# Optimization experiments

Hardware: AMD Instinct MI355X
Metric: run time of the kernel (lower is better)

Reference implementation:

```python
import jax, jax.numpy as jnp
import numpy as np

BEV_H, BEV_W = 50, 50
D_PILLAR = 4
PC = (-51.2, -51.2, -5.0, 51.2, 51.2, 3.0)
S_IMG = 518.0   # input_size; also img H and W used for uv normalization
LN_EPS = 1e-5
FUSE_EPS = 1e-6
C_CTX = 256


def _layernorm(x):
    mu = jnp.mean(x, axis=-1, keepdims=True)
    var = jnp.mean((x - mu) ** 2, axis=-1, keepdims=True)
    return (x - mu) * jax.lax.rsqrt(var + LN_EPS)


def _make_lidar2img(V):
    # realistic surround-view cameras: yaw-rotated extrinsics + pinhole intrinsics
    fx = fy = 400.0
    cx = cy = S_IMG / 2.0
    K = np.array([[fx, 0, cx, 0], [0, fy, cy, 0], [0, 0, 1, 0], [0, 0, 0, 1]], dtype=np.float64)
    mats = []
    for v in range(V):
        th = 2.0 * np.pi * v / V
        f = np.array([np.cos(th), np.sin(th), 0.0])      # camera forward (z)
        l = np.array([-np.sin(th), np.cos(th), 0.0])     # camera x (lateral)
        d = np.array([0.0, 0.0, -1.0])                   # camera y (down)
        R = np.stack([l, d, f], axis=0)
        t = np.array([0.0, 0.0, 1.5])                    # camera position in lidar frame
        E = np.eye(4); E[:3, :3] = R; E[:3, 3] = -R @ t
        mats.append(K @ E)
    return np.stack(mats, axis=0).astype(np.float32)     # (V,4,4)


def setup_inputs() -> dict:
    key = jax.random.key(0)
    k1, = jax.random.split(key, 1)
    B, V, N, C = 1, 6, 37 * 37, 768
    last_tokens = jax.random.normal(k1, (B, V, N, C), dtype=jnp.float32)
    lidar2img = jnp.asarray(_make_lidar2img(V))[None]    # (B,V,4,4)
    return {
        "last_tokens": last_tokens,
        "lidar2img": lidar2img,
        "w_view": jnp.zeros((1, V, 1), dtype=jnp.float32),
        "post_gamma": jnp.ones((C,), dtype=jnp.float32),
        "post_beta": jnp.zeros((C,), dtype=jnp.float32),
        "logits": jnp.zeros((C_CTX, C // C_CTX), dtype=jnp.float32),
        "patch_h": 37,
        "patch_w": 37,
    }


def _projection(lidar2img, dtype):
    # BEVFormer-style 3d reference points -> per-camera uv + visibility mask
    Z = int(round(PC[5] - PC[2]))  # 8
    zs = (jnp.linspace(0.5, Z - 0.5, D_PILLAR, dtype=dtype) / Z)[:, None, None]
    xs = (jnp.linspace(0.5, BEV_W - 0.5, BEV_W, dtype=dtype) / BEV_W)[None, None, :]
    ys = (jnp.linspace(0.5, BEV_H - 0.5, BEV_H, dtype=dtype) / BEV_H)[None, :, None]
    x, y, z = jnp.broadcast_arrays(xs, ys, zs)           # (D,H,W) each
    ref = jnp.stack([x, y, z], axis=-1).reshape(D_PILLAR, BEV_H * BEV_W, 3)
    ref = ref * jnp.array([PC[3] - PC[0], PC[4] - PC[1], PC[5] - PC[2]], dtype) \
        + jnp.array([PC[0], PC[1], PC[2]], dtype)
    ref4 = jnp.concatenate([ref, jnp.ones_like(ref[..., :1])], axis=-1)  # (D,Q,4)
    pts = jnp.einsum('bvij,dqj->bdvqi', lidar2img, ref4)  # (B,D,V,Q,4)
    zc = pts[..., 2]
    valid = zc > 1e-5
    uv = pts[..., :2] / jnp.maximum(zc, 1e-5)[..., None] / S_IMG
    u, v = uv[..., 0], uv[..., 1]
    valid = valid & (u > 0.0) & (u < 1.0) & (v > 0.0) & (v < 1.0)
    # -> (B,V,Q,D)
    tr = lambda a: jnp.transpose(a, (0, 2, 3, 1))
    return tr(u), tr(v), tr(valid)


def reference(last_tokens, lidar2img, w_view, post_gamma, post_beta, logits, patch_h, patch_w):
    B, V, N, C = last_tokens.shape
    Hp, Wp = int(patch_h), int(patch_w)
    Q = BEV_H * BEV_W
    dt = last_tokens.dtype

    # pre-LN over channels (no affine)
    tok = _layernorm(last_tokens)                         # (B,V,N,C)

    u, v, valid = _projection(lidar2img, dt)              # (B,V,Q,D)
    u, v = jax.lax.stop_gradient(u), jax.lax.stop_gradient(v)  # torch: @no_grad

    # pixel coords on the patch grid (align_corners=True grid_sample equivalent)
    x_p = (u * S_IMG + 0.5) / S_IMG * Wp - 0.5
    y_p = (v * S_IMG + 0.5) / S_IMG * Hp - 0.5

    x0 = jnp.floor(x_p); fx = x_p - x0; x0 = x0.astype(jnp.int32)
    y0 = jnp.floor(y_p); fy = y_p - y0; y0 = y0.astype(jnp.int32)

    QD = Q * D_PILLAR
    acc = jnp.zeros((B, V, QD, C), dtype=dt)
    for dx in (0, 1):
        for dy in (0, 1):
            xi, yi = x0 + dx, y0 + dy
            inb = (xi >= 0) & (xi < Wp) & (yi >= 0) & (yi < Hp)  # zeros padding
            w = jnp.where(dx, fx, 1.0 - fx) * jnp.where(dy, fy, 1.0 - fy) * inb.astype(dt)
            idx = jnp.clip(yi, 0, Hp - 1) * Wp + jnp.clip(xi, 0, Wp - 1)
            g = jnp.take_along_axis(tok, idx.reshape(B, V, QD, 1), axis=2)  # (B,V,QD,C)
            acc = acc + w.reshape(B, V, QD, 1) * g
    sampled = acc.reshape(B, V, Q, D_PILLAR, C)

    m = valid.astype(dt)                                  # (B,V,Q,D)
    feat = jnp.einsum('bvqdc,bvqd->bvqc', sampled, m)     # mask-weighted sum over pillar pts
    cnt = jnp.sum(m, axis=-1)                             # (B,V,Q)

    wv = jax.nn.softplus(w_view)                          # (1,V,1) positive per-view weights
    num = jnp.sum(feat * wv[..., None], axis=1)           # (B,Q,C)
    den = jnp.sum(cnt * wv, axis=1)                       # (B,Q)
    fused = num / (den[..., None] + FUSE_EPS)

    h = _layernorm(fused) * post_gamma + post_beta        # post-LN with affine

    g = C // C_CTX
    wg = jax.nn.softmax(logits, axis=-1)                  # (C_CTX, g)
    y = jnp.sum(h.reshape(B, Q, C_CTX, g) * wg[None, None], axis=-1)  # (B,Q,C_CTX)

    return jnp.transpose(y.reshape(B, BEV_H, BEV_W, C_CTX), (0, 3, 1, 2))
```

## Files before the change

### kernel.cpp

```cpp
#include <hip/hip_runtime.h>
#include <math.h>

#define NV      6
#define ND      4
#define NQ      2500
#define NPATCH  1369
#define NROWS   (NV * NPATCH)
#define CTOK    768
#define HP      37
#define WP      37
#define CCTX    256
#define QT      4
#define MAXM    96

__device__ __forceinline__ float softplus_f(float x) {
    return (x > 20.0f) ? x : log1pf(expf(x));
}

__global__ __launch_bounds__(256) void ln_stats_kernel(
    const float* __restrict__ tok, float* __restrict__ stats )
{
    const int wave = threadIdx.x >> 6, lane = threadIdx.x & 63;
    const int row = blockIdx.x * 4 + wave;
    if (row >= NROWS) return;
    const float4* x = (const float4*)(tok + (size_t)row * CTOK);
    float s = 0.f, ss = 0.f;
    #pragma unroll
    for (int i = 0; i < 3; ++i) {
        float4 v = x[lane + 64 * i];
        s  += (v.x + v.y) + (v.z + v.w);
        ss += v.x * v.x + v.y * v.y + v.z * v.z + v.w * v.w;
    }
    #pragma unroll
    for (int off = 32; off; off >>= 1) {
        s  += __shfl_down(s,  off, 64);
        ss += __shfl_down(ss, off, 64);
    }
    if (lane == 0) {
        float mu  = s * (1.0f / (float)CTOK);
        float var = ss * (1.0f / (float)CTOK) - mu * mu;
        float rs  = rsqrtf(fmaxf(var, 0.0f) + 1e-5f);
        stats[row * 2 + 0] = mu;
        stats[row * 2 + 1] = rs;
    }
}

__global__ __launch_bounds__(256) void bev_fuse_kernel(
    const float* __restrict__ tok,
    const float* __restrict__ stats,
    const float* __restrict__ lidar2img,
    const float* __restrict__ w_view,
    const float* __restrict__ gamma,
    const float* __restrict__ beta,
    const float* __restrict__ logits,
    float* __restrict__ out)
{
    __shared__ float s_b[QT][MAXM];
    __shared__ float s_bmu[QT][MAXM];
    __shared__ int   s_idx[QT][MAXM];
    __shared__ float s_den[QT][NV * ND];
    __shared__ int   s_cnt[QT];
    __shared__ float s_y[QT][CCTX];

    const int t = threadIdx.x;
    const int q0 = blockIdx.x * QT;

    if (t < QT) s_cnt[t] = 0;
    __syncthreads();

    if (t < QT * NV * ND) {
        const int qi = t / 24;
        const int p  = t - qi * 24;
        const int v = p >> 2, d = p & 3;
        const int q = q0 + qi;
        const int qy = q / 50, qx = q - qy * 50;
        float xf = ((float)qx + 0.5f) * (1.0f / 50.0f);
        float yf = ((float)qy + 0.5f) * (1.0f / 50.0f);
        float zf = (0.5f + (float)d * (7.0f / 3.0f)) * (1.0f / 8.0f);
        float X = xf * 102.4f - 51.2f;
        float Y = yf * 102.4f - 51.2f;
        float Z = zf * 8.0f - 5.0f;
        const float* M = lidar2img + v * 16;
        float px = M[0] * X + M[1] * Y + M[2]  * Z + M[3];
        float py = M[4] * X + M[5] * Y + M[6]  * Z + M[7];
        float pz = M[8] * X + M[9] * Y + M[10] * Z + M[11];
        bool valid = pz > 1e-5f;
        float zc = fmaxf(pz, 1e-5f);
        float uu = px / zc * (1.0f / 518.0f);
        float vv = py / zc * (1.0f / 518.0f);
        valid = valid && (uu > 0.0f) && (uu < 1.0f) && (vv > 0.0f) && (vv < 1.0f);

        float wv = softplus_f(w_view[v]);
        s_den[qi][p] = valid ? wv : 0.0f;

        if (valid) {
            float x_p = (uu * 518.0f + 0.5f) * (37.0f / 518.0f) - 0.5f;
            float y_p = (vv * 518.0f + 0.5f) * (37.0f / 518.0f) - 0.5f;
            float x0f = floorf(x_p), y0f = floorf(y_p);
            float fx = x_p - x0f, fy = y_p - y0f;
            int x0 = (int)x0f, y0 = (int)y0f;
            #pragma unroll
            for (int corner = 0; corner < 4; ++corner) {
                int dx = corner & 1, dy = corner >> 1;
                int xi = x0 + dx, yi = y0 + dy;
                bool inb = (xi >= 0) && (xi < WP) && (yi >= 0) && (yi < HP);
                float w = (dx ? fx : (1.0f - fx)) * (dy ? fy : (1.0f - fy));
                if (inb && w != 0.0f) {
                    int idx = v * NPATCH + yi * WP + xi;
                    float b = w * wv * stats[idx * 2 + 1];
                    int slot = atomicAdd(&s_cnt[qi], 1);
                    s_b[qi][slot]   = b;
                    s_bmu[qi][slot] = b * stats[idx * 2 + 0];
                    s_idx[qi][slot] = idx;
                }
            }
        }
    }
    __syncthreads();

    const int w = t >> 6, lane = t & 63;
    const int m = s_cnt[w];

    float den = 0.0f;
    #pragma unroll
    for (int p = 0; p < NV * ND; ++p) den += s_den[w][p];
    float c0 = 0.0f;
    for (int j = 0; j < m; ++j) c0 += s_bmu[w][j];

    const float4* base = (const float4*)tok;
    const int fp = 3 * lane;
    float4 a0 = {0,0,0,0}, a1 = {0,0,0,0}, a2 = {0,0,0,0};
    int j = 0;
    for (; j + 2 <= m; j += 2) {
        float b0 = s_b[w][j], b1 = s_b[w][j + 1];
        const float4* p0 = base + (size_t)s_idx[w][j]     * (CTOK / 4) + fp;
        const float4* p1 = base + (size_t)s_idx[w][j + 1] * (CTOK / 4) + fp;
        float4 x0 = p0[0], x1 = p0[1], x2 = p0[2];
        float4 y0 = p1[0], y1 = p1[1], y2 = p1[2];
        a0.x = fmaf(b0, x0.x, a0.x); a0.y = fmaf(b0, x0.y, a0.y);
        a0.z = fmaf(b0, x0.z, a0.z); a0.w = fmaf(b0, x0.w, a0.w);
        a1.x = fmaf(b0, x1.x, a1.x); a1.y = fmaf(b0, x1.y, a1.y);
        a1.z = fmaf(b0, x1.z, a1.z); a1.w = fmaf(b0, x1.w, a1.w);
        a2.x = fmaf(b0, x2.x, a2.x); a2.y = fmaf(b0, x2.y, a2.y);
        a2.z = fmaf(b0, x2.z, a2.z); a2.w = fmaf(b0, x2.w, a2.w);
        a0.x = fmaf(b1, y0.x, a0.x); a0.y = fmaf(b1, y0.y, a0.y);
        a0.z = fmaf(b1, y0.z, a0.z); a0.w = fmaf(b1, y0.w, a0.w);
        a1.x = fmaf(b1, y1.x, a1.x); a1.y = fmaf(b1, y1.y, a1.y);
        a1.z = fmaf(b1, y1.z, a1.z); a1.w = fmaf(b1, y1.w, a1.w);
        a2.x = fmaf(b1, y2.x, a2.x); a2.y = fmaf(b1, y2.y, a2.y);
        a2.z = fmaf(b1, y2.z, a2.z); a2.w = fmaf(b1, y2.w, a2.w);
    }
    if (j < m) {
        float b0 = s_b[w][j];
        const float4* p0 = base + (size_t)s_idx[w][j] * (CTOK / 4) + fp;
        float4 x0 = p0[0], x1 = p0[1], x2 = p0[2];
        a0.x = fmaf(b0, x0.x, a0.x); a0.y = fmaf(b0, x0.y, a0.y);
        a0.z = fmaf(b0, x0.z, a0.z); a0.w = fmaf(b0, x0.w, a0.w);
        a1.x = fmaf(b0, x1.x, a1.x); a1.y = fmaf(b0, x1.y, a1.y);
        a1.z = fmaf(b0, x1.z, a1.z); a1.w = fmaf(b0, x1.w, a1.w);
        a2.x = fmaf(b0, x2.x, a2.x); a2.y = fmaf(b0, x2.y, a2.y);
        a2.z = fmaf(b0, x2.z, a2.z); a2.w = fmaf(b0, x2.w, a2.w);
    }

    float f[12];
    {
        float inv = 1.0f / (den + 1e-6f);
        f[0]  = (a0.x - c0) * inv; f[1]  = (a0.y - c0) * inv;
        f[2]  = (a0.z - c0) * inv; f[3]  = (a0.w - c0) * inv;
        f[4]  = (a1.x - c0) * inv; f[5]  = (a1.y - c0) * inv;
        f[6]  = (a1.z - c0) * inv; f[7]  = (a1.w - c0) * inv;
        f[8]  = (a2.x - c0) * inv; f[9]  = (a2.y - c0) * inv;
        f[10] = (a2.z - c0) * inv; f[11] = (a2.w - c0) * inv;
    }

    float s = 0.f, ss = 0.f;
    #pragma unroll
    for (int i = 0; i < 12; ++i) { s += f[i]; ss += f[i] * f[i]; }
    #pragma unroll
    for (int off = 32; off; off >>= 1) {
        s  += __shfl_down(s,  off, 64);
        ss += __shfl_down(ss, off, 64);
    }
    s  = __shfl(s,  0, 64);
    ss = __shfl(ss, 0, 64);
    float mu  = s * (1.0f / (float)CTOK);
    float var = ss * (1.0f / (float)CTOK) - mu * mu;
    float rs  = rsqrtf(fmaxf(var, 0.0f) + 1e-5f);

    const float4* g4 = (const float4*)gamma;
    const float4* b4 = (const float4*)beta;
    float4 gv[3] = {g4[fp], g4[fp + 1], g4[fp + 2]};
    float4 bv[3] = {b4[fp], b4[fp + 1], b4[fp + 2]};
    const float* gs = (const float*)gv;
    const float* bs = (const float*)bv;
    float h[12];
    #pragma unroll
    for (int i = 0; i < 12; ++i)
        h[i] = (f[i] - mu) * rs * gs[i] + bs[i];

    const float4* lg4 = (const float4*)logits;
    float4 Lv[3] = {lg4[fp], lg4[fp + 1], lg4[fp + 2]};
    const float* lgv = (const float*)Lv;
    #pragma unroll
    for (int jj = 0; jj < 4; ++jj) {
        float l0 = lgv[jj * 3], l1 = lgv[jj * 3 + 1], l2 = lgv[jj * 3 + 2];
        float mx = fmaxf(l0, fmaxf(l1, l2));
        float e0 = expf(l0 - mx), e1 = expf(l1 - mx), e2 = expf(l2 - mx);
        float einv = 1.0f / (e0 + e1 + e2);
        s_y[w][lane * 4 + jj] =
            (h[jj * 3] * e0 + h[jj * 3 + 1] * e1 + h[jj * 3 + 2] * e2) * einv;
    }
    __syncthreads();

    float4 o;
    o.x = s_y[0][t]; o.y = s_y[1][t]; o.z = s_y[2][t]; o.w = s_y[3][t];
    *(float4*)(out + (size_t)t * NQ + q0) = o;
}

extern "C" void kernel_launch(void* const* d_in, const int* in_sizes, int n_in,
                              void* d_out, int out_size, void* d_ws, size_t ws_size,
                              hipStream_t stream) {
    const float* last_tokens = (const float*)d_in[0];
    const float* lidar2img   = (const float*)d_in[1];
    const float* w_view      = (const float*)d_in[2];
    const float* post_gamma  = (const float*)d_in[3];
    const float* post_beta   = (const float*)d_in[4];
    const float* logits      = (const float*)d_in[5];
    float* out = (float*)d_out;

    float* stats = (float*)d_ws;

    ln_stats_kernel<<<(NROWS + 3) / 4, 256, 0, stream>>>(last_tokens, stats);
    bev_fuse_kernel<<<NQ / QT, 256, 0, stream>>>(last_tokens, stats, lidar2img,
                                                 w_view, post_gamma, post_beta,
                                                 logits, out);
}
```

Baseline: 98.68 us.

## Fuse per-token LayerNorm statistics into the gather loop, drop stats kernel

```diff
diff --git a/kernel.cpp b/kernel.cpp
--- a/kernel.cpp
+++ b/kernel.cpp
@@ -5,7 +5,6 @@
 #define ND      4
 #define NQ      2500
 #define NPATCH  1369
-#define NROWS   (NV * NPATCH)
 #define CTOK    768
 #define HP      37
 #define WP      37
@@ -17,37 +16,8 @@
     return (x > 20.0f) ? x : log1pf(expf(x));
 }
 
-__global__ __launch_bounds__(256) void ln_stats_kernel(
-    const float* __restrict__ tok, float* __restrict__ stats )
-{
-    const int wave = threadIdx.x >> 6, lane = threadIdx.x & 63;
-    const int row = blockIdx.x * 4 + wave;
-    if (row >= NROWS) return;
-    const float4* x = (const float4*)(tok + (size_t)row * CTOK);
-    float s = 0.f, ss = 0.f;
-    #pragma unroll
-    for (int i = 0; i < 3; ++i) {
-        float4 v = x[lane + 64 * i];
-        s  += (v.x + v.y) + (v.z + v.w);
-        ss += v.x * v.x + v.y * v.y + v.z * v.z + v.w * v.w;
-    }
-    #pragma unroll
-    for (int off = 32; off; off >>= 1) {
-        s  += __shfl_down(s,  off, 64);
-        ss += __shfl_down(ss, off, 64);
-    }
-    if (lane == 0) {
-        float mu  = s * (1.0f / (float)CTOK);
-        float var = ss * (1.0f / (float)CTOK) - mu * mu;
-        float rs  = rsqrtf(fmaxf(var, 0.0f) + 1e-5f);
-        stats[row * 2 + 0] = mu;
-        stats[row * 2 + 1] = rs;
-    }
-}
-
 __global__ __launch_bounds__(256) void bev_fuse_kernel(
     const float* __restrict__ tok,
-    const float* __restrict__ stats,
     const float* __restrict__ lidar2img,
     const float* __restrict__ w_view,
     const float* __restrict__ gamma,
@@ -56,7 +26,6 @@
     float* __restrict__ out)
 {
     __shared__ float s_b[QT][MAXM];
-    __shared__ float s_bmu[QT][MAXM];
     __shared__ int   s_idx[QT][MAXM];
     __shared__ float s_den[QT][NV * ND];
     __shared__ int   s_cnt[QT];
@@ -106,12 +75,9 @@
                 bool inb = (xi >= 0) && (xi < WP) && (yi >= 0) && (yi < HP);
                 float w = (dx ? fx : (1.0f - fx)) * (dy ? fy : (1.0f - fy));
                 if (inb && w != 0.0f) {
-                    int idx = v * NPATCH + yi * WP + xi;
-                    float b = w * wv * stats[idx * 2 + 1];
                     int slot = atomicAdd(&s_cnt[qi], 1);
-                    s_b[qi][slot]   = b;
-                    s_bmu[qi][slot] = b * stats[idx * 2 + 0];
-                    s_idx[qi][slot] = idx;
+                    s_b[qi][slot]   = w * wv;
+                    s_idx[qi][slot] = v * NPATCH + yi * WP + xi;
                 }
             }
         }
@@ -124,19 +90,44 @@
     float den = 0.0f;
     #pragma unroll
     for (int p = 0; p < NV * ND; ++p) den += s_den[w][p];
-    float c0 = 0.0f;
-    for (int j = 0; j < m; ++j) c0 += s_bmu[w][j];
 
     const float4* base = (const float4*)tok;
     const int fp = 3 * lane;
     float4 a0 = {0,0,0,0}, a1 = {0,0,0,0}, a2 = {0,0,0,0};
+    float c0 = 0.0f;
     int j = 0;
     for (; j + 2 <= m; j += 2) {
-        float b0 = s_b[w][j], b1 = s_b[w][j + 1];
+        float wb0 = s_b[w][j], wb1 = s_b[w][j + 1];
         const float4* p0 = base + (size_t)s_idx[w][j]     * (CTOK / 4) + fp;
         const float4* p1 = base + (size_t)s_idx[w][j + 1] * (CTOK / 4) + fp;
         float4 x0 = p0[0], x1 = p0[1], x2 = p0[2];
         float4 y0 = p1[0], y1 = p1[1], y2 = p1[2];
+        float sA  = ((x0.x + x0.y) + (x0.z + x0.w)) + ((x1.x + x1.y) + (x1.z + x1.w))
+                  + ((x2.x + x2.y) + (x2.z + x2.w));
+        float ssA = x0.x*x0.x + x0.y*x0.y + x0.z*x0.z + x0.w*x0.w
+                  + x1.x*x1.x + x1.y*x1.y + x1.z*x1.z + x1.w*x1.w
+                  + x2.x*x2.x + x2.y*x2.y + x2.z*x2.z + x2.w*x2.w;
+        float sB  = ((y0.x + y0.y) + (y0.z + y0.w)) + ((y1.x + y1.y) + (y1.z + y1.w))
+                  + ((y2.x + y2.y) + (y2.z + y2.w));
+        float ssB = y0.x*y0.x + y0.y*y0.y + y0.z*y0.z + y0.w*y0.w
+                  + y1.x*y1.x + y1.y*y1.y + y1.z*y1.z + y1.w*y1.w
+                  + y2.x*y2.x + y2.y*y2.y + y2.z*y2.z + y2.w*y2.w;
+        #pragma unroll
+        for (int off = 32; off; off >>= 1) {
+            sA  += __shfl_xor(sA,  off, 64);
+            ssA += __shfl_xor(ssA, off, 64);
+            sB  += __shfl_xor(sB,  off, 64);
+            ssB += __shfl_xor(ssB, off, 64);
+        }
+        float muA  = sA * (1.0f / (float)CTOK);
+        float varA = ssA * (1.0f / (float)CTOK) - muA * muA;
+        float rsA  = rsqrtf(fmaxf(varA, 0.0f) + 1e-5f);
+        float muB  = sB * (1.0f / (float)CTOK);
+        float varB = ssB * (1.0f / (float)CTOK) - muB * muB;
+        float rsB  = rsqrtf(fmaxf(varB, 0.0f) + 1e-5f);
+        float b0 = wb0 * rsA, b1 = wb1 * rsB;
+        c0 = fmaf(b0, muA, c0);
+        c0 = fmaf(b1, muB, c0);
         a0.x = fmaf(b0, x0.x, a0.x); a0.y = fmaf(b0, x0.y, a0.y);
         a0.z = fmaf(b0, x0.z, a0.z); a0.w = fmaf(b0, x0.w, a0.w);
         a1.x = fmaf(b0, x1.x, a1.x); a1.y = fmaf(b0, x1.y, a1.y);
@@ -151,9 +142,24 @@
         a2.z = fmaf(b1, y2.z, a2.z); a2.w = fmaf(b1, y2.w, a2.w);
     }
     if (j < m) {
-        float b0 = s_b[w][j];
+        float wb0 = s_b[w][j];
         const float4* p0 = base + (size_t)s_idx[w][j] * (CTOK / 4) + fp;
         float4 x0 = p0[0], x1 = p0[1], x2 = p0[2];
+        float sA  = ((x0.x + x0.y) + (x0.z + x0.w)) + ((x1.x + x1.y) + (x1.z + x1.w))
+                  + ((x2.x + x2.y) + (x2.z + x2.w));
+        float ssA = x0.x*x0.x + x0.y*x0.y + x0.z*x0.z + x0.w*x0.w
+                  + x1.x*x1.x + x1.y*x1.y + x1.z*x1.z + x1.w*x1.w
+                  + x2.x*x2.x + x2.y*x2.y + x2.z*x2.z + x2.w*x2.w;
+        #pragma unroll
+        for (int off = 32; off; off >>= 1) {
+            sA  += __shfl_xor(sA,  off, 64);
+            ssA += __shfl_xor(ssA, off, 64);
+        }
+        float muA  = sA * (1.0f / (float)CTOK);
+        float varA = ssA * (1.0f / (float)CTOK) - muA * muA;
+        float rsA  = rsqrtf(fmaxf(varA, 0.0f) + 1e-5f);
+        float b0 = wb0 * rsA;
+        c0 = fmaf(b0, muA, c0);
         a0.x = fmaf(b0, x0.x, a0.x); a0.y = fmaf(b0, x0.y, a0.y);
         a0.z = fmaf(b0, x0.z, a0.z); a0.w = fmaf(b0, x0.w, a0.w);
         a1.x = fmaf(b0, x1.x, a1.x); a1.y = fmaf(b0, x1.y, a1.y);
@@ -178,11 +184,9 @@
     for (int i = 0; i < 12; ++i) { s += f[i]; ss += f[i] * f[i]; }
     #pragma unroll
     for (int off = 32; off; off >>= 1) {
-        s  += __shfl_down(s,  off, 64);
-        ss += __shfl_down(ss, off, 64);
-    }
-    s  = __shfl(s,  0, 64);
-    ss = __shfl(ss, 0, 64);
+        s  += __shfl_xor(s,  off, 64);
+        ss += __shfl_xor(ss, off, 64);
+    }
     float mu  = s * (1.0f / (float)CTOK);
     float var = ss * (1.0f / (float)CTOK) - mu * mu;
     float rs  = rsqrtf(fmaxf(var, 0.0f) + 1e-5f);
@@ -228,10 +232,7 @@
     const float* logits      = (const float*)d_in[5];
     float* out = (float*)d_out;
 
-    float* stats = (float*)d_ws;
-
-    ln_stats_kernel<<<(NROWS + 3) / 4, 256, 0, stream>>>(last_tokens, stats);
-    bev_fuse_kernel<<<NQ / QT, 256, 0, stream>>>(last_tokens, stats, lidar2img,
+    bev_fuse_kernel<<<NQ / QT, 256, 0, stream>>>(last_tokens, lidar2img,
                                                  w_view, post_gamma, post_beta,
                                                  logits, out);
 }
```

Result: slower. 100.7 us (+2.1%).
